# Performance work log

Measured on AMD Instinct MI355X. Metric: run time of the kernel, lower is better.

The kernel has to match this reference:

```python
import jax, jax.numpy as jnp
import numpy as np

RECON_W = 0.1
CONT_W = 0.2
EPS = 1e-7  # BCE log clamp (torch clamps log at -100; eps-clip is the jax analogue)


def setup_inputs() -> dict:
    key = jax.random.key(0)
    k1, k2, k3, k4 = jax.random.split(key, 4)
    B, M = 256, 4096
    predictions = jax.random.uniform(k1, (B, M, 9), dtype=jnp.float32)
    targets = jax.random.uniform(k2, (B, M, 9), dtype=jnp.float32)
    reconstructed = jax.random.normal(k3, (B, 1, 128, 128), dtype=jnp.float32)
    images = jax.random.normal(k4, (B, 1, 128, 128), dtype=jnp.float32)
    return {"predictions": predictions, "targets": targets,
            "reconstructed": reconstructed, "images": images}


def _continuity_loss(p3, valid_mask):
    # p3: [B, M, 2]; valid_mask: [B, M] bool
    # For each valid slot i, find the next valid slot j > i and accumulate
    # mean(|p3[i] - p3[j]|) -- vectorized replacement for the ragged double loop.
    B, M, _ = p3.shape
    idx = jnp.arange(M, dtype=jnp.int32)
    BIG = jnp.int32(M)
    pos = jnp.where(valid_mask, idx[None, :], BIG)              # [B, M]
    # suffix min over j >= i of pos, then shift to get strict j > i
    suf = jnp.flip(jax.lax.cummin(jnp.flip(pos, axis=1), axis=1), axis=1)
    nxt = jnp.concatenate([suf[:, 1:], jnp.full((B, 1), BIG, jnp.int32)], axis=1)
    pair_valid = valid_mask & (nxt < BIG)                       # [B, M]
    nxt_c = jnp.clip(nxt, 0, M - 1)
    p3_next = jnp.take_along_axis(p3, nxt_c[..., None], axis=1)  # [B, M, 2]
    dist = jnp.abs(p3 - p3_next).mean(axis=-1)                  # [B, M]
    return jnp.sum(dist * pair_valid.astype(p3.dtype)) / B


def _loss(predictions, targets, reconstructed, images):
    target_curves = targets[..., :8]
    target_validity = targets[..., 8:9]
    valid_mask = target_validity[..., 0] > 0.5                  # [B, M]
    fmask = valid_mask.astype(predictions.dtype)
    n_valid = jnp.sum(fmask)

    def masked_l1(pred, tgt, width):
        num = jnp.sum(jnp.abs(pred - tgt) * fmask[..., None])
        return jnp.where(n_valid > 0, num / jnp.maximum(n_valid * width, 1.0), 0.0)

    coord_loss = masked_l1(predictions[..., :6], target_curves[..., :6], 6.0)
    width_loss = masked_l1(predictions[..., 6:8], target_curves[..., 6:8], 2.0)

    p = jnp.clip(predictions[..., 8:9], EPS, 1.0 - EPS)
    t = target_validity
    validity_loss = jnp.mean(-(t * jnp.log(p) + (1.0 - t) * jnp.log(1.0 - p)))

    continuity_loss = _continuity_loss(predictions[..., 4:6], valid_mask)
    reconstruction_loss = jnp.mean((reconstructed - images) ** 2)

    total = (coord_loss + width_loss + 2.0 * validity_loss
             + CONT_W * continuity_loss + RECON_W * reconstruction_loss)
    return total


def reference(predictions, targets, reconstructed, images):
    return _loss(predictions, targets, reconstructed, images)
```

## Files before the change

### kernel.cpp

```cpp
#include <hip/hip_runtime.h>
#include <math.h>

#define B_DIM 256
#define M_DIM 4096
#define EPSV 1e-7f
#define THREADS 1024
#define NWAVES (THREADS / 64)
#define WAVE_ELEMS (M_DIM / NWAVES)
#define SUB 64
#define NSUB (WAVE_ELEMS / SUB)
#define SUB_F4 (SUB * 9 / 4)
#define WAVE_F4 (WAVE_ELEMS * 9 / 4)
#define ROW_F4 (M_DIM * 9 / 4)
#define RECON_F4_PER_BLOCK ((B_DIM * 128 * 128 / 4) / B_DIM)


#define LOADW(cc, P0, P1, P2, T0, T1, T2)                              \
    do {                                                               \
        const float4* pc_ = pw + (cc) * SUB_F4;                        \
        const float4* tc_ = tw + (cc) * SUB_F4;                        \
        P0 = pc_[lane];      T0 = tc_[lane];                           \
        P1 = pc_[lane + 64]; T1 = tc_[lane + 64];                      \
        if (lane < 16) { P2 = pc_[lane + 128]; T2 = tc_[lane + 128]; } \
    } while (0)

#define STOREW(P0, P1, P2, T0, T1, T2)                                 \
    do {                                                               \
        float4* sp_ = (float4*)(s_stage[wave]);                        \
        float4* st_ = (float4*)(s_stage[wave] + 576);                  \
        sp_[lane] = P0;      st_[lane] = T0;                           \
        sp_[lane + 64] = P1; st_[lane + 64] = T1;                      \
        if (lane < 16) { sp_[lane + 128] = P2; st_[lane + 128] = T2; } \
    } while (0)

__global__ void __launch_bounds__(THREADS)
__attribute__((amdgpu_waves_per_eu(4, 4)))
fused_loss_kernel(
    const float4* __restrict__ pred4, const float4* __restrict__ tgt4,
    const float4* __restrict__ rec4, const float4* __restrict__ img4,
    float* __restrict__ blk_out)
{
    __shared__ float s_stage[NWAVES][1152];
    __shared__ float s_p4[M_DIM];
    __shared__ float s_p5[M_DIM];
    __shared__ unsigned long long s_words[M_DIM / 64];
    __shared__ float s_red[16][6];

    const int b    = blockIdx.x;
    const int t    = threadIdx.x;
    const int lane = t & 63;
    const int wave = t >> 6;

    const float4* pw = pred4 + (size_t)b * ROW_F4 + wave * WAVE_F4;
    const float4* tw = tgt4  + (size_t)b * ROW_F4 + wave * WAVE_F4;

    float coord_s = 0.f, width_s = 0.f, val_s = 0.f, nval_s = 0.f;

    auto consume = [&](int c) {
        const float* pe = s_stage[wave] + lane * 9;
        const float* te = s_stage[wave] + 576 + lane * 9;
        float p0 = pe[0], p1 = pe[1], p2 = pe[2], p3 = pe[3], p4 = pe[4],
              p5 = pe[5], p6 = pe[6], p7 = pe[7], p8 = pe[8];
        float t0 = te[0], t1 = te[1], t2 = te[2], t3 = te[3], t4 = te[4],
              t5 = te[5], t6 = te[6], t7 = te[7], t8 = te[8];

        bool valid = (t8 > 0.5f);
        float fm = valid ? 1.f : 0.f;
        coord_s += fm * (fabsf(p0 - t0) + fabsf(p1 - t1) + fabsf(p2 - t2) +
                         fabsf(p3 - t3) + fabsf(p4 - t4) + fabsf(p5 - t5));
        width_s += fm * (fabsf(p6 - t6) + fabsf(p7 - t7));
        nval_s  += fm;

        float pc8 = fminf(fmaxf(p8, EPSV), 1.0f - EPSV);
        val_s += -(t8 * __logf(pc8) + (1.0f - t8) * __logf(1.0f - pc8));

        const int m = wave * WAVE_ELEMS + c * SUB + lane;
        s_p4[m] = p4;
        s_p5[m] = p5;
        unsigned long long bal = __ballot(valid);
        if (lane == 0) s_words[wave * NSUB + c] = bal;
    };

    float4 PA0, PA1, PA2, TA0, TA1, TA2;
    float4 PB0, PB1, PB2, TB0, TB1, TB2;

    LOADW(0, PA0, PA1, PA2, TA0, TA1, TA2);

    float recon_s = 0.f;
    {
        const float4* rb = rec4 + (size_t)b * RECON_F4_PER_BLOCK;
        const float4* ib = img4 + (size_t)b * RECON_F4_PER_BLOCK;
        #pragma unroll
        for (int i = 0; i < RECON_F4_PER_BLOCK / THREADS; ++i) {
            int idx = i * THREADS + t;
            float4 r = rb[idx]; float4 m = ib[idx];
            float d0 = r.x - m.x, d1 = r.y - m.y, d2 = r.z - m.z, d3 = r.w - m.w;
            recon_s += d0 * d0 + d1 * d1 + d2 * d2 + d3 * d3;
        }
    }

    STOREW(PA0, PA1, PA2, TA0, TA1, TA2);
    LOADW(1, PB0, PB1, PB2, TB0, TB1, TB2);
    consume(0);

    STOREW(PB0, PB1, PB2, TB0, TB1, TB2);
    LOADW(2, PA0, PA1, PA2, TA0, TA1, TA2);
    consume(1);

    STOREW(PA0, PA1, PA2, TA0, TA1, TA2);
    LOADW(3, PB0, PB1, PB2, TB0, TB1, TB2);
    consume(2);

    STOREW(PB0, PB1, PB2, TB0, TB1, TB2);
    consume(3);

    __syncthreads();

    float cont_s = 0.f;
    #pragma unroll
    for (int p = 0; p < 4; ++p) {
        const int m   = p * 1024 + t;
        const int w   = m >> 6;
        const int bit = m & 63;
        unsigned long long wv = s_words[w];
        if ((wv >> bit) & 1ULL) {
            unsigned long long mask = wv & ((bit == 63) ? 0ULL : (~0ULL << (bit + 1)));
            int nxt = -1;
            if (mask) {
                nxt = (w << 6) + __builtin_ctzll(mask);
            } else {
                for (int w2 = w + 1; w2 < (M_DIM / 64); ++w2) {
                    unsigned long long mw = s_words[w2];
                    if (mw) { nxt = (w2 << 6) + __builtin_ctzll(mw); break; }
                }
            }
            if (nxt >= 0) {
                cont_s += 0.5f * (fabsf(s_p4[m] - s_p4[nxt]) +
                                  fabsf(s_p5[m] - s_p5[nxt]));
            }
        }
    }

    float vals[6] = {coord_s, width_s, val_s, nval_s, cont_s, recon_s};
    #pragma unroll
    for (int i = 0; i < 6; ++i) {
        float v = vals[i];
        #pragma unroll
        for (int off = 32; off > 0; off >>= 1) v += __shfl_down(v, off, 64);
        vals[i] = v;
    }
    if (lane == 0) {
        #pragma unroll
        for (int i = 0; i < 6; ++i) s_red[wave][i] = vals[i];
    }
    __syncthreads();
    if (t == 0) {
        float acc[6] = {0.f, 0.f, 0.f, 0.f, 0.f, 0.f};
        for (int wv = 0; wv < 16; ++wv)
            #pragma unroll
            for (int i = 0; i < 6; ++i) acc[i] += s_red[wv][i];
        float* r = blk_out + b * 8;
        #pragma unroll
        for (int i = 0; i < 6; ++i) r[i] = acc[i];
    }
}

__global__ __launch_bounds__(256) void finalize_kernel(
    const float* __restrict__ ws, float* __restrict__ out)
{
    const int t = threadIdx.x;
    const float* rb = ws + t * 8;
    float v[6];
    #pragma unroll
    for (int i = 0; i < 6; ++i) v[i] = rb[i];

    __shared__ float sred[4][6];
    int lane = t & 63, wave = t >> 6;
    #pragma unroll
    for (int i = 0; i < 6; ++i) {
        float x = v[i];
        #pragma unroll
        for (int off = 32; off > 0; off >>= 1) x += __shfl_down(x, off, 64);
        v[i] = x;
    }
    if (lane == 0)
        #pragma unroll
        for (int i = 0; i < 6; ++i) sred[wave][i] = v[i];
    __syncthreads();
    if (t == 0) {
        double a[6];
        #pragma unroll
        for (int i = 0; i < 6; ++i)
            a[i] = (double)sred[0][i] + (double)sred[1][i] +
                   (double)sred[2][i] + (double)sred[3][i];
        double coord_num = a[0], width_num = a[1], val_sum = a[2],
               nv = a[3], cont = a[4], recon = a[5];

        double coord = (nv > 0.0) ? coord_num / fmax(nv * 6.0, 1.0) : 0.0;
        double width = (nv > 0.0) ? width_num / fmax(nv * 2.0, 1.0) : 0.0;
        double validity = val_sum / ((double)B_DIM * (double)M_DIM);
        double contl    = cont / (double)B_DIM;
        double reconl   = recon / ((double)B_DIM * 128.0 * 128.0);

        out[0] = (float)(coord + width + 2.0 * validity +
                         0.2 * contl + 0.1 * reconl);
    }
}

extern "C" void kernel_launch(void* const* d_in, const int* in_sizes, int n_in,
                              void* d_out, int out_size, void* d_ws, size_t ws_size,
                              hipStream_t stream) {
    const float* pred = (const float*)d_in[0];
    const float* tgt  = (const float*)d_in[1];
    const float* rec  = (const float*)d_in[2];
    const float* img  = (const float*)d_in[3];
    float* ws = (float*)d_ws;

    fused_loss_kernel<<<B_DIM, THREADS, 0, stream>>>(
        (const float4*)pred, (const float4*)tgt,
        (const float4*)rec, (const float4*)img, ws);
    finalize_kernel<<<1, 256, 0, stream>>>(ws, (float*)d_out);
}
```

Before: 132.4 us.

## Replace LDS-staged coalesced loads with direct strided per-element global loads

```diff
diff --git a/kernel.cpp b/kernel.cpp
--- a/kernel.cpp
+++ b/kernel.cpp
@@ -5,42 +5,17 @@
 #define M_DIM 4096
 #define EPSV 1e-7f
 #define THREADS 1024
-#define NWAVES (THREADS / 64)
-#define WAVE_ELEMS (M_DIM / NWAVES)
-#define SUB 64
-#define NSUB (WAVE_ELEMS / SUB)
-#define SUB_F4 (SUB * 9 / 4)
-#define WAVE_F4 (WAVE_ELEMS * 9 / 4)
-#define ROW_F4 (M_DIM * 9 / 4)
+#define ROW_ELEMS (M_DIM * 9)
 #define RECON_F4_PER_BLOCK ((B_DIM * 128 * 128 / 4) / B_DIM)
 
 
-#define LOADW(cc, P0, P1, P2, T0, T1, T2)                              \
-    do {                                                               \
-        const float4* pc_ = pw + (cc) * SUB_F4;                        \
-        const float4* tc_ = tw + (cc) * SUB_F4;                        \
-        P0 = pc_[lane];      T0 = tc_[lane];                           \
-        P1 = pc_[lane + 64]; T1 = tc_[lane + 64];                      \
-        if (lane < 16) { P2 = pc_[lane + 128]; T2 = tc_[lane + 128]; } \
-    } while (0)
-
-#define STOREW(P0, P1, P2, T0, T1, T2)                                 \
-    do {                                                               \
-        float4* sp_ = (float4*)(s_stage[wave]);                        \
-        float4* st_ = (float4*)(s_stage[wave] + 576);                  \
-        sp_[lane] = P0;      st_[lane] = T0;                           \
-        sp_[lane + 64] = P1; st_[lane + 64] = T1;                      \
-        if (lane < 16) { sp_[lane + 128] = P2; st_[lane + 128] = T2; } \
-    } while (0)
 
 __global__ void __launch_bounds__(THREADS)
-__attribute__((amdgpu_waves_per_eu(4, 4)))
 fused_loss_kernel(
-    const float4* __restrict__ pred4, const float4* __restrict__ tgt4,
+    const float* __restrict__ pred, const float* __restrict__ tgt,
     const float4* __restrict__ rec4, const float4* __restrict__ img4,
     float* __restrict__ blk_out)
 {
-    __shared__ float s_stage[NWAVES][1152];
     __shared__ float s_p4[M_DIM];
     __shared__ float s_p5[M_DIM];
     __shared__ unsigned long long s_words[M_DIM / 64];
@@ -51,40 +26,8 @@
     const int lane = t & 63;
     const int wave = t >> 6;
 
-    const float4* pw = pred4 + (size_t)b * ROW_F4 + wave * WAVE_F4;
-    const float4* tw = tgt4  + (size_t)b * ROW_F4 + wave * WAVE_F4;
-
-    float coord_s = 0.f, width_s = 0.f, val_s = 0.f, nval_s = 0.f;
-
-    auto consume = [&](int c) {
-        const float* pe = s_stage[wave] + lane * 9;
-        const float* te = s_stage[wave] + 576 + lane * 9;
-        float p0 = pe[0], p1 = pe[1], p2 = pe[2], p3 = pe[3], p4 = pe[4],
-              p5 = pe[5], p6 = pe[6], p7 = pe[7], p8 = pe[8];
-        float t0 = te[0], t1 = te[1], t2 = te[2], t3 = te[3], t4 = te[4],
-              t5 = te[5], t6 = te[6], t7 = te[7], t8 = te[8];
-
-        bool valid = (t8 > 0.5f);
-        float fm = valid ? 1.f : 0.f;
-        coord_s += fm * (fabsf(p0 - t0) + fabsf(p1 - t1) + fabsf(p2 - t2) +
-                         fabsf(p3 - t3) + fabsf(p4 - t4) + fabsf(p5 - t5));
-        width_s += fm * (fabsf(p6 - t6) + fabsf(p7 - t7));
-        nval_s  += fm;
-
-        float pc8 = fminf(fmaxf(p8, EPSV), 1.0f - EPSV);
-        val_s += -(t8 * __logf(pc8) + (1.0f - t8) * __logf(1.0f - pc8));
-
-        const int m = wave * WAVE_ELEMS + c * SUB + lane;
-        s_p4[m] = p4;
-        s_p5[m] = p5;
-        unsigned long long bal = __ballot(valid);
-        if (lane == 0) s_words[wave * NSUB + c] = bal;
-    };
-
-    float4 PA0, PA1, PA2, TA0, TA1, TA2;
-    float4 PB0, PB1, PB2, TB0, TB1, TB2;
-
-    LOADW(0, PA0, PA1, PA2, TA0, TA1, TA2);
+    const float* pb = pred + (size_t)b * ROW_ELEMS;
+    const float* tb = tgt  + (size_t)b * ROW_ELEMS;
 
     float recon_s = 0.f;
     {
@@ -99,20 +42,39 @@
         }
     }
 
-    STOREW(PA0, PA1, PA2, TA0, TA1, TA2);
-    LOADW(1, PB0, PB1, PB2, TB0, TB1, TB2);
-    consume(0);
+    float coord_s = 0.f, width_s = 0.f, val_s = 0.f, nval_s = 0.f;
 
-    STOREW(PB0, PB1, PB2, TB0, TB1, TB2);
-    LOADW(2, PA0, PA1, PA2, TA0, TA1, TA2);
-    consume(1);
+    #pragma unroll
+    for (int c = 0; c < 4; ++c) {
+        const int m = c * 1024 + t;
+        const float* pe = pb + (size_t)m * 9;
+        const float* te = tb + (size_t)m * 9;
 
-    STOREW(PA0, PA1, PA2, TA0, TA1, TA2);
-    LOADW(3, PB0, PB1, PB2, TB0, TB1, TB2);
-    consume(2);
+        float4 pA, pB; float p8;
+        float4 tA, tB; float t8;
+        __builtin_memcpy(&pA, pe,     16);
+        __builtin_memcpy(&pB, pe + 4, 16);
+        p8 = pe[8];
+        __builtin_memcpy(&tA, te,     16);
+        __builtin_memcpy(&tB, te + 4, 16);
+        t8 = te[8];
 
-    STOREW(PB0, PB1, PB2, TB0, TB1, TB2);
-    consume(3);
+        bool valid = (t8 > 0.5f);
+        float fm = valid ? 1.f : 0.f;
+        coord_s += fm * (fabsf(pA.x - tA.x) + fabsf(pA.y - tA.y) +
+                         fabsf(pA.z - tA.z) + fabsf(pA.w - tA.w) +
+                         fabsf(pB.x - tB.x) + fabsf(pB.y - tB.y));
+        width_s += fm * (fabsf(pB.z - tB.z) + fabsf(pB.w - tB.w));
+        nval_s  += fm;
+
+        float pc8 = fminf(fmaxf(p8, EPSV), 1.0f - EPSV);
+        val_s += -(t8 * __logf(pc8) + (1.0f - t8) * __logf(1.0f - pc8));
+
+        s_p4[m] = pB.x;
+        s_p5[m] = pB.y;
+        unsigned long long bal = __ballot(valid);
+        if (lane == 0) s_words[c * 16 + wave] = bal;
+    }
 
     __syncthreads();
 
@@ -217,7 +179,6 @@
     float* ws = (float*)d_ws;
 
     fused_loss_kernel<<<B_DIM, THREADS, 0, stream>>>(
-        (const float4*)pred, (const float4*)tgt,
-        (const float4*)rec, (const float4*)img, ws);
+        pred, tgt, (const float4*)rec, (const float4*)img, ws);
     finalize_kernel<<<1, 256, 0, stream>>>(ws, (float*)d_out);
 }
```

Result: no change. 132.7 us (+0.3%).
